# Kernel optimization log

Measured on AMD Instinct MI355X. Metric: run time of the kernel, lower is better.

## Reference

```python
import jax, jax.numpy as jnp
import numpy as np


def setup_inputs() -> dict:
    key = jax.random.key(0)
    k1, k2 = jax.random.split(key)
    B, C, H, W = 8, 19, 512, 512
    logits = jax.random.normal(k1, (B, C, H, W), dtype=jnp.float32)
    labels = jax.random.randint(k2, (B, H, W), 0, C, dtype=jnp.int64)
    return {"logits": logits, "labels": labels}


def _lovasz_softmax_flat(probs_flat, labels_flat, C):
    # probs_flat: [N, C], labels_flat: [N]
    def per_class(pc, c):
        # pc: [N] probabilities for class c
        fg = (labels_flat == c).astype(pc.dtype)          # [N]
        errors = jnp.abs(fg - pc)                          # [N]
        order = jnp.argsort(-errors)                       # descending sort
        errors_sorted = errors[order]
        fg_sorted = fg[order]
        gts = fg_sorted.sum()
        intersection = gts - jnp.cumsum(fg_sorted)
        union = gts + jnp.cumsum(1.0 - fg_sorted)
        jaccard = 1.0 - intersection / union
        # first-difference: jaccard[1:] -= jaccard[:-1]
        jaccard = jnp.concatenate([jaccard[:1], jaccard[1:] - jaccard[:-1]])
        return jnp.dot(errors_sorted, jaccard), gts > 0

    losses, present = jax.vmap(per_class)(probs_flat.T, jnp.arange(C))
    # torch code skips absent classes; emulate with masked mean
    n_present = jnp.maximum(jnp.sum(present.astype(losses.dtype)), 1.0)
    return jnp.sum(jnp.where(present, losses, 0.0)) / n_present


def reference(logits, labels):
    probs = jax.nn.softmax(logits, axis=1)                 # [B,C,H,W]
    B, C, H, W = probs.shape
    probs_flat = jnp.transpose(probs, (0, 2, 3, 1)).reshape(-1, C)  # [N,C]
    labels_flat = labels.reshape(-1)                       # [N]
    return _lovasz_softmax_flat(probs_flat, labels_flat, C)
```

## Files before the change

kernel.cpp:

```cpp
#include <hip/hip_runtime.h>

#define NB     128
#define NCLS   19
#define HW     (512*512)
#define NPIX   (8*HW)
#define HSZ    (NCLS*NB)
#define NMID   64
#define NBLK   2048

__global__ __launch_bounds__(256) void hist_kernel(const float* __restrict__ logits,
                                                   const int* __restrict__ labels,
                                                   unsigned* __restrict__ partials) {
    __shared__ unsigned h[HSZ];
    for (int i = threadIdx.x; i < HSZ; i += 256) h[i] = 0u;
    __syncthreads();

    int gt = blockIdx.x * 256 + threadIdx.x;
    const int stride = NBLK * 256;
#pragma unroll
    for (int it = 0; it < NPIX / (2 * stride); ++it) {
        int p0 = (gt + it * stride) * 2;
        int b  = p0 >> 18;
        int hw = p0 & (HW - 1);
        const float* base = logits + ((size_t)b * NCLS) * HW + hw;

        float e0[NCLS], e1[NCLS];
        float s0 = 0.f, s1 = 0.f;
#pragma unroll
        for (int c = 0; c < NCLS; ++c) {
            float2 z = *(const float2*)(base + (size_t)c * HW);
            z.x = __expf(z.x);
            z.y = __expf(z.y);
            e0[c] = z.x; e1[c] = z.y;
            s0 += z.x; s1 += z.y;
        }
        float sc0 = (float)(NB - 1) * __builtin_amdgcn_rcpf(s0);
        float sc1 = (float)(NB - 1) * __builtin_amdgcn_rcpf(s1);
        int2 lb = *(const int2*)(labels + p0);

#pragma unroll
        for (int c = 0; c < NCLS; ++c) {
            float t0 = fmaf(e0[c], sc0, 0.5f);
            bool  f0 = (lb.x == c);
            t0 = f0 ? ((float)NB - t0) : t0;
            atomicAdd(&h[c * NB + (int)t0], f0 ? 0x10000u : 1u);

            float t1 = fmaf(e1[c], sc1, 0.5f);
            bool  f1 = (lb.y == c);
            t1 = f1 ? ((float)NB - t1) : t1;
            atomicAdd(&h[c * NB + (int)t1], f1 ? 0x10000u : 1u);
        }
    }

    __syncthreads();
    unsigned* out = partials + (size_t)blockIdx.x * HSZ;
    for (int i = threadIdx.x; i < HSZ; i += 256) out[i] = h[i];
}

__global__ __launch_bounds__(128) void mid_kernel(const unsigned* __restrict__ partials,
                                                  unsigned* __restrict__ mid_lo,
                                                  unsigned* __restrict__ mid_hi,
                                                  unsigned* __restrict__ lock,
                                                  unsigned long long* __restrict__ acc,
                                                  unsigned* __restrict__ npres) {
    if (blockIdx.x == 0 && blockIdx.y == 0 && threadIdx.x == 0) {
        *lock = 0u; *acc = 0ull; *npres = 0u;
    }
    int idx = blockIdx.x * 128 + threadIdx.x;
    int y = blockIdx.y;
    const int per = NBLK / NMID;
    unsigned lo = 0, hi = 0;
#pragma unroll 4
    for (int k = 0; k < per; ++k) {
        unsigned v = partials[(size_t)(y * per + k) * HSZ + idx];
        lo += v & 0xFFFFu;
        hi += v >> 16;
    }
    mid_lo[y * HSZ + idx] = lo;
    mid_hi[y * HSZ + idx] = hi;
}

__global__ __launch_bounds__(128) void scan_kernel(const unsigned* __restrict__ mid_lo,
                                                   const unsigned* __restrict__ mid_hi,
                                                   unsigned* __restrict__ lock,
                                                   unsigned long long* __restrict__ acc,
                                                   unsigned* __restrict__ npres,
                                                   float* __restrict__ out) {
    int c = blockIdx.x;
    int t = threadIdx.x;
    int bkt = NB - 1 - t;

    unsigned lo = 0, hi = 0;
#pragma unroll 8
    for (int y = 0; y < NMID; ++y) {
        lo += mid_lo[y * HSZ + c * NB + bkt];
        hi += mid_hi[y * HSZ + c * NB + bkt];
    }
    long long n_t = (long long)lo + (long long)hi;
    long long f_t = (long long)hi;

    __shared__ long long sn[NB], sf[NB];
    __shared__ long long totf;
    sn[t] = n_t; sf[t] = f_t;
    __syncthreads();
    if (t == 0) {
        long long an = 0, af = 0;
        for (int k = 0; k < NB; ++k) {
            long long nn = sn[k], ff = sf[k];
            sn[k] = an; sf[k] = af;
            an += nn; af += ff;
        }
        totf = af;
    }
    __syncthreads();
    long long g = totf;

    double loss_t = 0.0;
    if (g > 0 && n_t > 0) {
        long long i  = sn[t], F  = sf[t];
        long long i2 = i + n_t, F2 = F + f_t;
        double Jp = 1.0 - (double)(g - F)  / (double)(g + i  - F);
        double Jn = 1.0 - (double)(g - F2) / (double)(g + i2 - F2);
        loss_t = ((double)bkt * (1.0 / (double)(NB - 1))) * (Jn - Jp);
    }

    __shared__ double sl[NB];
    sl[t] = loss_t;
    __syncthreads();
    for (int off = NB / 2; off > 0; off >>= 1) {
        if (t < off) sl[t] += sl[t + off];
        __syncthreads();
    }

    if (t == 0) {
        if (g > 0) {
            unsigned long long q =
                (unsigned long long)(long long)(sl[0] * 9007199254740992.0);
            atomicAdd(acc, q);
            atomicAdd(npres, 1u);
        }
        __threadfence();
        unsigned old = atomicAdd(lock, 1u);
        if (old == NCLS - 1) {
            unsigned long long a = atomicAdd(acc, 0ull);
            unsigned np = atomicAdd(npres, 0u);
            double s = (double)(long long)a * (1.0 / 9007199254740992.0);
            out[0] = (float)(s / (double)(np ? np : 1u));
        }
    }
}

extern "C" void kernel_launch(void* const* d_in, const int* in_sizes, int n_in,
                              void* d_out, int out_size, void* d_ws, size_t ws_size,
                              hipStream_t stream) {
    const float* logits = (const float*)d_in[0];
    const int*   labels = (const int*)d_in[1];
    float* out = (float*)d_out;

    unsigned* partials = (unsigned*)d_ws;
    unsigned* mid_lo = partials + (size_t)NBLK * HSZ;
    unsigned* mid_hi = mid_lo + (size_t)NMID * HSZ;
    unsigned long long* acc =
        (unsigned long long*)(((uintptr_t)(mid_hi + (size_t)NMID * HSZ) + 15) & ~(uintptr_t)15);
    unsigned* lock  = (unsigned*)(acc + 1);
    unsigned* npres = lock + 1;

    hist_kernel<<<NBLK, 256, 0, stream>>>(logits, labels, partials);
    mid_kernel<<<dim3(HSZ / 128, NMID), 128, 0, stream>>>(partials, mid_lo, mid_hi,
                                                          lock, acc, npres);
    scan_kernel<<<NCLS, NB, 0, stream>>>(mid_lo, mid_hi, lock, acc, npres, out);
}
```

Baseline: 49.67 us.

## Merge block histograms via atomics into 64 copies and drop mid reduction kernel

Each histogram block now atomically adds its shared-memory histogram, skipping zero bins, into one of 64 global copies chosen by block index. Previously every block wrote a full partial histogram to global memory and a separate mid kernel reduced them. This removes roughly 20 MB of partial-histogram writes and reads plus one reduction pass, while the scan kernel unpacks the packed counts itself. In exchange it adds a small zeroing kernel and global atomic contention, and it relies on the 16-bit packed count fields not overflowing, since each copy holds 32 blocks.

```diff
diff --git a/kernel.cpp b/kernel.cpp
--- a/kernel.cpp
+++ b/kernel.cpp
@@ -5,12 +5,21 @@
 #define HW     (512*512)
 #define NPIX   (8*HW)
 #define HSZ    (NCLS*NB)
-#define NMID   64
+#define NCOPY  64
 #define NBLK   2048
+
+__global__ __launch_bounds__(256) void zero_kernel(unsigned* __restrict__ copies,
+                                                   unsigned long long* __restrict__ acc,
+                                                   unsigned* __restrict__ lock,
+                                                   unsigned* __restrict__ npres) {
+    int i = blockIdx.x * 256 + threadIdx.x;
+    copies[i] = 0u;
+    if (i == 0) { *acc = 0ull; *lock = 0u; *npres = 0u; }
+}
 
 __global__ __launch_bounds__(256) void hist_kernel(const float* __restrict__ logits,
                                                    const int* __restrict__ labels,
-                                                   unsigned* __restrict__ partials) {
+                                                   unsigned* __restrict__ copies) {
     __shared__ unsigned h[HSZ];
     for (int i = threadIdx.x; i < HSZ; i += 256) h[i] = 0u;
     __syncthreads();
@@ -53,35 +62,14 @@
     }
 
     __syncthreads();
-    unsigned* out = partials + (size_t)blockIdx.x * HSZ;
-    for (int i = threadIdx.x; i < HSZ; i += 256) out[i] = h[i];
+    unsigned* dst = copies + (size_t)(blockIdx.x & (NCOPY - 1)) * HSZ;
+    for (int i = threadIdx.x; i < HSZ; i += 256) {
+        unsigned v = h[i];
+        if (v) atomicAdd(&dst[i], v);
+    }
 }
 
-__global__ __launch_bounds__(128) void mid_kernel(const unsigned* __restrict__ partials,
-                                                  unsigned* __restrict__ mid_lo,
-                                                  unsigned* __restrict__ mid_hi,
-                                                  unsigned* __restrict__ lock,
-                                                  unsigned long long* __restrict__ acc,
-                                                  unsigned* __restrict__ npres) {
-    if (blockIdx.x == 0 && blockIdx.y == 0 && threadIdx.x == 0) {
-        *lock = 0u; *acc = 0ull; *npres = 0u;
-    }
-    int idx = blockIdx.x * 128 + threadIdx.x;
-    int y = blockIdx.y;
-    const int per = NBLK / NMID;
-    unsigned lo = 0, hi = 0;
-#pragma unroll 4
-    for (int k = 0; k < per; ++k) {
-        unsigned v = partials[(size_t)(y * per + k) * HSZ + idx];
-        lo += v & 0xFFFFu;
-        hi += v >> 16;
-    }
-    mid_lo[y * HSZ + idx] = lo;
-    mid_hi[y * HSZ + idx] = hi;
-}
-
-__global__ __launch_bounds__(128) void scan_kernel(const unsigned* __restrict__ mid_lo,
-                                                   const unsigned* __restrict__ mid_hi,
+__global__ __launch_bounds__(128) void scan_kernel(const unsigned* __restrict__ copies,
                                                    unsigned* __restrict__ lock,
                                                    unsigned long long* __restrict__ acc,
                                                    unsigned* __restrict__ npres,
@@ -92,9 +80,10 @@
 
     unsigned lo = 0, hi = 0;
 #pragma unroll 8
-    for (int y = 0; y < NMID; ++y) {
-        lo += mid_lo[y * HSZ + c * NB + bkt];
-        hi += mid_hi[y * HSZ + c * NB + bkt];
+    for (int y = 0; y < NCOPY; ++y) {
+        unsigned v = copies[y * HSZ + c * NB + bkt];
+        lo += v & 0xFFFFu;
+        hi += v >> 16;
     }
     long long n_t = (long long)lo + (long long)hi;
     long long f_t = (long long)hi;
@@ -157,16 +146,13 @@
     const int*   labels = (const int*)d_in[1];
     float* out = (float*)d_out;
 
-    unsigned* partials = (unsigned*)d_ws;
-    unsigned* mid_lo = partials + (size_t)NBLK * HSZ;
-    unsigned* mid_hi = mid_lo + (size_t)NMID * HSZ;
+    unsigned* copies = (unsigned*)d_ws;
     unsigned long long* acc =
-        (unsigned long long*)(((uintptr_t)(mid_hi + (size_t)NMID * HSZ) + 15) & ~(uintptr_t)15);
+        (unsigned long long*)(((uintptr_t)(copies + (size_t)NCOPY * HSZ) + 15) & ~(uintptr_t)15);
     unsigned* lock  = (unsigned*)(acc + 1);
     unsigned* npres = lock + 1;
 
-    hist_kernel<<<NBLK, 256, 0, stream>>>(logits, labels, partials);
-    mid_kernel<<<dim3(HSZ / 128, NMID), 128, 0, stream>>>(partials, mid_lo, mid_hi,
-                                                          lock, acc, npres);
-    scan_kernel<<<NCLS, NB, 0, stream>>>(mid_lo, mid_hi, lock, acc, npres, out);
+    zero_kernel<<<(NCOPY * HSZ) / 256, 256, 0, stream>>>(copies, acc, lock, npres);
+    hist_kernel<<<NBLK, 256, 0, stream>>>(logits, labels, copies);
+    scan_kernel<<<NCLS, NB, 0, stream>>>(copies, lock, acc, npres, out);
 }
```

Result: no change. 49.68 us (+0.0%).
